# Kernel tuning notes

Hardware: AMD Instinct MI355X
Metric: run time of the kernel (lower is better)

## Reference

```python
import jax, jax.numpy as jnp
import numpy as np

B, C, H, W = 8, 64, 256, 256
V = H * W
E = (H - 1) * W + H * (W - 1)  # vertical + horizontal grid edges
N_ROUNDS = int(np.ceil(np.log2(V)))  # Boruvka halves #components per round


def build_index():
    # matches _build_matrix_index: raw_index[y, x] = y * W + x
    raw = jnp.arange(V, dtype=jnp.int32).reshape(H, W)
    row_e = jnp.stack([raw[:-1, :], raw[1:, :]], axis=-1).reshape(-1, 2)  # vertical edges
    col_e = jnp.stack([raw[:, :-1], raw[:, 1:]], axis=-1).reshape(-1, 2)  # horizontal edges
    return jnp.concatenate([row_e, col_e], axis=0)  # [E, 2]


def edge_weights(fm):
    # distance_func = squared L2 over channel dim; weight = dist + 1 (so weight >= 1)
    b = fm.shape[0]
    d_row = ((fm[:, :, :-1, :] - fm[:, :, 1:, :]) ** 2).sum(1).reshape(b, -1)
    d_col = ((fm[:, :, :, :-1] - fm[:, :, :, 1:]) ** 2).sum(1).reshape(b, -1)
    return jnp.concatenate([d_row, d_col], axis=1) + 1.0  # [B, E]


def mst_boruvka(u, v, w):
    """Parallel Boruvka MST on a connected graph. u, v: [E] int32, w: [E] float32.
    Returns boolean selection mask over edges (exactly V-1 True)."""
    eidx = jnp.arange(E, dtype=jnp.int32)
    vidx = jnp.arange(V, dtype=jnp.int32)
    INF = jnp.float32(jnp.inf)
    BIG = jnp.int32(E)  # sentinel edge id

    def round_fn(state, _):
        comp, sel = state
        cu, cv = comp[u], comp[v]
        active = cu != cv
        wa = jnp.where(active, w, INF)
        # min outgoing edge weight per component
        minw = jnp.full((V,), INF, jnp.float32).at[cu].min(wa).at[cv].min(wa)
        # tie-break by smallest edge index (consistent tie-break -> no long cycles)
        cand_u = jnp.where(active & (wa == minw[cu]), eidx, BIG)
        cand_v = jnp.where(active & (wa == minw[cv]), eidx, BIG)
        best = jnp.full((V,), BIG, jnp.int32).at[cu].min(cand_u).at[cv].min(cand_v)
        has = best < BIG
        be = jnp.clip(best, 0, E - 1)
        cu_b, cv_b = comp[u[be]], comp[v[be]]
        # hook each component onto the component at the other end of its best edge
        parent = jnp.where(has, jnp.where(cu_b == vidx, cv_b, cu_b), vidx)
        # break mutual 2-cycles: keep the smaller label as root
        pp = parent[parent]
        parent = jnp.where((pp == vidx) & (vidx < parent), vidx, parent)
        # pointer jumping to full path compression
        for _ in range(N_ROUNDS):
            parent = parent[parent]
        comp = parent[comp]
        sel = sel.at[jnp.where(has, best, BIG)].set(True, mode='drop')
        return (comp, sel), None

    init = (vidx, jnp.zeros((E,), dtype=bool))
    (comp, sel), _ = jax.lax.scan(round_fn, init, None, length=N_ROUNDS)
    return sel


def setup_inputs() -> dict:
    key = jax.random.key(0)
    guide_in = jax.random.normal(key, (B, C, H, W), dtype=jnp.float32)
    return {"guide_in": guide_in}


def reference(guide_in):
    index = build_index()                      # [E, 2] shared across batch
    weight = edge_weights(guide_in)            # [B, E]
    u, v = index[:, 0], index[:, 1]
    sel = jax.vmap(lambda wb: mst_boruvka(u, v, wb))(weight)  # [B, E] bool
    # grid graph is connected -> exactly V-1 MST edges per image (static shape)
    eids = jax.vmap(lambda s: jnp.nonzero(s, size=V - 1, fill_value=0)[0])(sel)
    tree = index[eids]                         # [B, V-1, 2] vertex pairs of the MST
    return tree
```

## Files before the change

kernel.cpp:

```cpp
#include <hip/hip_runtime.h>
#include <stdint.h>

typedef unsigned long long ull;

#define Bc 8
#define Cc 64
#define Hc 256
#define Wc 256
#define Vc (Hc*Wc)
#define REc ((Hc-1)*Wc)
#define Ec (REc + Hc*(Wc-1))
#define VM1 (Vc-1)
#define INF64 0xFFFFFFFFFFFFFFFFull
#define NRND 16
#define EPB 8192
#define BPB 16

__device__ __forceinline__ void edge_uv(int e, int& u, int& v){
  if (e < REc){ u = e; v = e + Wc; }
  else { int k = e - REc; int i = k / (Wc-1); int j = k - i*(Wc-1); u = i*Wc + j; v = u + 1; }
}

__device__ __forceinline__ ull packw(float w, int e){
  return ((ull)__float_as_uint(w) << 32) | (unsigned)e;
}

__device__ __forceinline__ int chase(const int* __restrict__ parB, int x){
  int p = parB[x];
  while (p != x){ x = p; p = parB[x]; }
  return x;
}

__global__ void __launch_bounds__(1024)
k_weights(const float* __restrict__ g, float* __restrict__ wf,
          int* __restrict__ L, int* __restrict__ par,
          ull* __restrict__ b0, ull* __restrict__ b1,
          unsigned char* __restrict__ sel, int* __restrict__ act, int* __restrict__ outp){
  int t = blockIdx.x*1024 + threadIdx.x;
  int b = t >> 16; int v = t & VM1;
  int i = v >> 8, j = v & (Wc-1);
  const bool hU = i > 0, hD = i < Hc-1, hL = j > 0, hR = j < Wc-1;
  const int oU = hU ? -Wc : 0, oD = hD ? Wc : 0, oL = hL ? -1 : 0, oR = hR ? 1 : 0;
  const float* p = g + (size_t)b*Cc*Vc + v;
  float sU = 0.f, sD = 0.f, sL = 0.f, sR = 0.f;
  #pragma unroll 4
  for (int c = 0; c < Cc; ++c){
    const float* pc = p + (size_t)c*Vc;
    float x = pc[0];
    float dU = x - pc[oU];  float dD = x - pc[oD];
    float dL = x - pc[oL];  float dR = x - pc[oR];
    sU += dU*dU; sD += dD*dD; sL += dL*dL; sR += dR*dR;
  }
  float wU = sU + 1.0f, wD = sD + 1.0f, wL = sL + 1.0f, wR = sR + 1.0f;
  int eU = v - Wc, eD = v, eL = REc + i*(Wc-1) + j - 1, eR = REc + i*(Wc-1) + j;
  ull m = INF64;
  if (hU){ ull x = packw(wU, eU); if (x < m) m = x; }
  if (hD){ ull x = packw(wD, eD); if (x < m) m = x; }
  if (hL){ ull x = packw(wL, eL); if (x < m) m = x; }
  if (hR){ ull x = packw(wR, eR); if (x < m) m = x; }
  b0[t] = m;
  b1[t] = INF64;
  L[t] = v; par[t] = v;
  float* wfb = wf + (size_t)b*Ec;
  unsigned char* selb = sel + (size_t)b*Ec;
  if (hD){ wfb[eD] = wD; selb[eD] = 0; }
  if (hR){ wfb[eR] = wR; selb[eR] = 0; }
  if (t < Bc*VM1){ outp[2*t] = 0; outp[2*t+1] = Wc; }
  if (t < (NRND+2)*Bc) act[t] = 0;
}

__global__ void __launch_bounds__(1024)
k_scanmerge(const float* __restrict__ wf, int* __restrict__ L,
            const int* __restrict__ par,
            ull* __restrict__ bcur, ull* __restrict__ bnxt,
            const int* __restrict__ act, int r){
  int t = blockIdx.x*1024 + threadIdx.x;
  int b = t >> 16;
  if (!act[r*Bc + b]) return;
  int v = t & VM1; const int base = b << 16;
  const int* parB = par + base;
  int Lt0 = L[t];
  int i = v >> 8, j = v & (Wc-1);
  int Lu = (i > 0)    ? L[base + v - Wc] : Lt0;
  int Ld = (i < Hc-1) ? L[base + v + Wc] : Lt0;
  int Ll = (j > 0)    ? L[base + v - 1 ] : Lt0;
  int Lr = (j < Wc-1) ? L[base + v + 1 ] : Lt0;
  if ((Lu==Lt0) & (Ld==Lt0) & (Ll==Lt0) & (Lr==Lt0)){
    if (Lt0 != v) return;
    if (parB[v] == v){ bnxt[t] = INF64; return; }
  }
  int rt = chase(parB, Lt0);
  if (rt != Lt0) L[t] = rt;
  if (v == rt) bnxt[t] = INF64;
  const float* wfb = wf + (size_t)b*Ec;
  ull m = INF64;
  if (Lu != Lt0 && Lu != rt && chase(parB, Lu) != rt){
    int e = v - Wc; ull x = packw(wfb[e], e); if (x < m) m = x; }
  if (Ld != Lt0 && Ld != rt && chase(parB, Ld) != rt){
    int e = v;      ull x = packw(wfb[e], e); if (x < m) m = x; }
  if (Ll != Lt0 && Ll != rt && chase(parB, Ll) != rt){
    int e = REc + i*(Wc-1) + j - 1; ull x = packw(wfb[e], e); if (x < m) m = x; }
  if (Lr != Lt0 && Lr != rt && chase(parB, Lr) != rt){
    int e = REc + i*(Wc-1) + j;     ull x = packw(wfb[e], e); if (x < m) m = x; }
  if (m != INF64) atomicMin(&bcur[base + rt], m);
}

__global__ void __launch_bounds__(1024)
k_hook(const int* __restrict__ L, const ull* __restrict__ bcur,
       int* __restrict__ par, unsigned char* __restrict__ sel, int* __restrict__ act, int r){
  int t = blockIdx.x*1024 + threadIdx.x;
  int b = t >> 16;
  if (r > 0 && !act[r*Bc + b]) return;
  int v = t & VM1;
  if (L[t] != v) return;
  const int base = b << 16;
  ull p = bcur[t];
  int pr = v;
  if (p != INF64){
    int e = (int)(unsigned)p; int eu, ev; edge_uv(e, eu, ev);
    int cu = L[base + eu], cv = L[base + ev];
    int other = (cu == v) ? cv : cu;
    sel[(size_t)b*Ec + e] = 1;
    if (act[(r+1)*Bc + b] == 0) act[(r+1)*Bc + b] = 1;
    pr = (bcur[base + other] == p && v < other) ? v : other;
  }
  par[t] = pr;
}

__global__ void __launch_bounds__(1024)
k_cnt(const unsigned char* __restrict__ sel, int* __restrict__ blkcnt){
  int blk = blockIdx.x; int bb = blk / BPB; int kb = blk % BPB;
  int base = kb*EPB;
  int off = threadIdx.x * 8;
  int c = 0;
  if (base + off < Ec){
    const unsigned int* p = (const unsigned int*)(sel + (size_t)bb*Ec + base + off);
    unsigned int s = p[0] + p[1];
    c = (s & 0xFF) + ((s>>8)&0xFF) + ((s>>16)&0xFF) + (s>>24);
  }
  int lane = threadIdx.x & 63, wave = threadIdx.x >> 6;
  #pragma unroll
  for (int o = 32; o; o >>= 1) c += __shfl_down(c, o, 64);
  __shared__ int sw[16];
  if (lane == 0) sw[wave] = c;
  __syncthreads();
  if (threadIdx.x == 0){
    int s = 0;
    #pragma unroll
    for (int w = 0; w < 16; ++w) s += sw[w];
    blkcnt[blk] = s;
  }
}

__global__ void __launch_bounds__(1024)
k_scatter(const unsigned char* __restrict__ sel, const int* __restrict__ blkcnt,
          int* __restrict__ outp){
  int blk = blockIdx.x; int bb = blk / BPB; int kb = blk % BPB;
  __shared__ int s_boff;
  if (threadIdx.x < 64){
    int c = ((int)threadIdx.x < kb) ? blkcnt[bb*BPB + threadIdx.x] : 0;
    #pragma unroll
    for (int o = 32; o; o >>= 1) c += __shfl_down(c, o, 64);
    if (threadIdx.x == 0) s_boff = c;
  }
  int base = kb*EPB;
  int off = threadIdx.x * 8;
  unsigned int a = 0, d = 0; int c = 0;
  if (base + off < Ec){
    const unsigned int* p = (const unsigned int*)(sel + (size_t)bb*Ec + base + off);
    a = p[0]; d = p[1];
    unsigned int s = a + d;
    c = (s & 0xFF) + ((s>>8)&0xFF) + ((s>>16)&0xFF) + (s>>24);
  }
  int lane = threadIdx.x & 63, wave = threadIdx.x >> 6;
  int x = c;
  #pragma unroll
  for (int o = 1; o < 64; o <<= 1){ int y = __shfl_up(x, o, 64); if (lane >= o) x += y; }
  __shared__ int sw[16];
  if (lane == 63) sw[wave] = x;
  __syncthreads();
  int woff = 0;
  #pragma unroll
  for (int w = 0; w < 16; ++w) if (w < wave) woff += sw[w];
  int pos = s_boff + woff + x - c;
  if (base + off < Ec){
    int* ob = outp + (size_t)bb*VM1*2;
    int ebase = base + off;
    #pragma unroll
    for (int k = 0; k < 8; ++k){
      unsigned int byte = ((k < 4) ? (a >> (8*k)) : (d >> (8*(k-4)))) & 0xFF;
      if (byte){ int e = ebase + k; int u, v; edge_uv(e, u, v); ob[2*pos] = u; ob[2*pos+1] = v; ++pos; }
    }
  }
}

extern "C" void kernel_launch(void* const* d_in, const int* in_sizes, int n_in,
                              void* d_out, int out_size, void* d_ws, size_t ws_size,
                              hipStream_t stream) {
  const float* g = (const float*)d_in[0];
  int* outp = (int*)d_out;

  char* ws = (char*)d_ws;
  size_t off = 0;
  auto alloc = [&](size_t bytes) -> void* {
    void* p = ws + off; off += (bytes + 511) & ~(size_t)511; return p;
  };
  ull* b0 = (ull*)alloc((size_t)Bc*Vc*8);
  ull* b1 = (ull*)alloc((size_t)Bc*Vc*8);
  float* wf = (float*)alloc((size_t)Bc*Ec*4);
  int* L   = (int*)alloc((size_t)Bc*Vc*4);
  int* par = (int*)alloc((size_t)Bc*Vc*4);
  unsigned char* sel = (unsigned char*)alloc((size_t)Bc*Ec);
  int* act  = (int*)alloc((size_t)(NRND+2)*Bc*4);
  int* blkcnt = (int*)alloc((size_t)Bc*BPB*4);

  const int gv = (Bc*Vc)/1024;

  k_weights<<<gv, 1024, 0, stream>>>(g, wf, L, par, b0, b1, sel, act, outp);
  k_hook   <<<gv, 1024, 0, stream>>>(L, b0, par, sel, act, 0);
  for (int r = 1; r < NRND; ++r){
    ull* bcur = (r & 1) ? b1 : b0;
    ull* bnxt = (r & 1) ? b0 : b1;
    k_scanmerge<<<gv, 1024, 0, stream>>>(wf, L, par, bcur, bnxt, act, r);
    k_hook     <<<gv, 1024, 0, stream>>>(L, bcur, par, sel, act, r);
  }
  k_cnt    <<<Bc*BPB, 1024, 0, stream>>>(sel, blkcnt);
  k_scatter<<<Bc*BPB, 1024, 0, stream>>>(sel, blkcnt, outp);
}
```

Before: 248.3 us.

## Fuse edge weighting with tile-local Boruvka rounds in shared memory

Replaces the weight kernel and the first global hook with one kernel. Each 1024-thread block covers a 32x32 tile, computes its edge weights, then runs Boruvka rounds inside shared memory, hooking only when a component's minimum incident edge lies fully inside the tile. Each image enters the global scan/hook rounds with far fewer components, so those rounds do less pointer chasing and fewer atomics, and the act flags let idle rounds exit early. In exchange it adds up to 16 barrier-synchronised local rounds per block and more shared-memory traffic in the first kernel.

Result: faster. 240.8 us (-3.0%).

```diff
diff --git a/kernel.cpp b/kernel.cpp
--- a/kernel.cpp
+++ b/kernel.cpp
@@ -2,6 +2,7 @@
 #include <stdint.h>
 
 typedef unsigned long long ull;
+typedef unsigned short u16;
 
 #define Bc 8
 #define Cc 64
@@ -12,6 +13,7 @@
 #define Ec (REc + Hc*(Wc-1))
 #define VM1 (Vc-1)
 #define INF64 0xFFFFFFFFFFFFFFFFull
+#define TS 32
 #define NRND 16
 #define EPB 8192
 #define BPB 16
@@ -32,41 +34,95 @@
 }
 
 __global__ void __launch_bounds__(1024)
-k_weights(const float* __restrict__ g, float* __restrict__ wf,
-          int* __restrict__ L, int* __restrict__ par,
-          ull* __restrict__ b0, ull* __restrict__ b1,
-          unsigned char* __restrict__ sel, int* __restrict__ act, int* __restrict__ outp){
-  int t = blockIdx.x*1024 + threadIdx.x;
-  int b = t >> 16; int v = t & VM1;
-  int i = v >> 8, j = v & (Wc-1);
+k_stage1(const float* __restrict__ g, float* __restrict__ wf,
+         int* __restrict__ L, int* __restrict__ par, ull* __restrict__ b1,
+         unsigned char* __restrict__ sel, int* __restrict__ act, int* __restrict__ outp){
+  const int blk = blockIdx.x;
+  const int b = blk >> 6, tile = blk & 63;
+  const int ty = tile >> 3, tx = tile & 7;
+  const int tid = threadIdx.x;
+  const int li = tid >> 5, lj = tid & 31;
+  const int i = ty*TS + li, j = tx*TS + lj;
+  const int v = (i << 8) | j;
+
   const bool hU = i > 0, hD = i < Hc-1, hL = j > 0, hR = j < Wc-1;
   const int oU = hU ? -Wc : 0, oD = hD ? Wc : 0, oL = hL ? -1 : 0, oR = hR ? 1 : 0;
   const float* p = g + (size_t)b*Cc*Vc + v;
-  float sU = 0.f, sD = 0.f, sL = 0.f, sR = 0.f;
+  float sU=0.f, sD=0.f, sL=0.f, sR=0.f;
   #pragma unroll 4
   for (int c = 0; c < Cc; ++c){
     const float* pc = p + (size_t)c*Vc;
     float x = pc[0];
-    float dU = x - pc[oU];  float dD = x - pc[oD];
-    float dL = x - pc[oL];  float dR = x - pc[oR];
+    float dU = x - pc[oU]; float dD = x - pc[oD];
+    float dL = x - pc[oL]; float dR = x - pc[oR];
     sU += dU*dU; sD += dD*dD; sL += dL*dL; sR += dR*dR;
   }
-  float wU = sU + 1.0f, wD = sD + 1.0f, wL = sL + 1.0f, wR = sR + 1.0f;
-  int eU = v - Wc, eD = v, eL = REc + i*(Wc-1) + j - 1, eR = REc + i*(Wc-1) + j;
-  ull m = INF64;
-  if (hU){ ull x = packw(wU, eU); if (x < m) m = x; }
-  if (hD){ ull x = packw(wD, eD); if (x < m) m = x; }
-  if (hL){ ull x = packw(wL, eL); if (x < m) m = x; }
-  if (hR){ ull x = packw(wR, eR); if (x < m) m = x; }
-  b0[t] = m;
-  b1[t] = INF64;
-  L[t] = v; par[t] = v;
+  const int eU = v - Wc, eD = v, eL = REc + i*(Wc-1) + j - 1, eR = REc + i*(Wc-1) + j;
+  const ull pU = packw(sU+1.f, eU), pD = packw(sD+1.f, eD);
+  const ull pL = packw(sL+1.f, eL), pR = packw(sR+1.f, eR);
   float* wfb = wf + (size_t)b*Ec;
   unsigned char* selb = sel + (size_t)b*Ec;
-  if (hD){ wfb[eD] = wD; selb[eD] = 0; }
-  if (hR){ wfb[eR] = wR; selb[eR] = 0; }
-  if (t < Bc*VM1){ outp[2*t] = 0; outp[2*t+1] = Wc; }
-  if (t < (NRND+2)*Bc) act[t] = 0;
+  if (hD){ wfb[eD] = sD+1.f; selb[eD] = 0; }
+  if (hR){ wfb[eR] = sR+1.f; selb[eR] = 0; }
+  { int gt = blk*1024 + tid;
+    if (gt < Bc*VM1){ outp[2*gt] = 0; outp[2*gt+1] = Wc; }
+    if (gt < (NRND+2)*Bc) act[gt] = (gt >= Bc && gt < 2*Bc) ? 1 : 0;
+  }
+
+  __shared__ u16 lab[1024];
+  __shared__ u16 spar[1024];
+  __shared__ ull best[1024];
+  __shared__ int s_any;
+  lab[tid] = (u16)tid;
+
+  for (int round = 0; round < 16; ++round){
+    best[tid] = INF64;
+    if (tid == 0) s_any = 0;
+    __syncthreads();
+    int c = lab[tid];
+    ull m = INF64;
+    if (hU){ bool inc = (li > 0)    ? (lab[tid-TS] != c) : true; if (inc && pU < m) m = pU; }
+    if (hD){ bool inc = (li < TS-1) ? (lab[tid+TS] != c) : true; if (inc && pD < m) m = pD; }
+    if (hL){ bool inc = (lj > 0)    ? (lab[tid-1 ] != c) : true; if (inc && pL < m) m = pL; }
+    if (hR){ bool inc = (lj < TS-1) ? (lab[tid+1 ] != c) : true; if (inc && pR < m) m = pR; }
+    if (m != INF64) atomicMin(&best[c], m);
+    __syncthreads();
+    int pr = tid;
+    if (c == tid){
+      ull pb = best[tid];
+      if (pb != INF64){
+        int e = (int)(unsigned)pb; int eu, ev; edge_uv(e, eu, ev);
+        int diu = (eu>>8) - ty*TS, dju = (eu&255) - tx*TS;
+        int div_ = (ev>>8) - ty*TS, djv = (ev&255) - tx*TS;
+        bool inu  = ((unsigned)diu < TS) && ((unsigned)dju < TS);
+        bool inv_ = ((unsigned)div_ < TS) && ((unsigned)djv < TS);
+        if (inu && inv_){
+          int lu = diu*TS + dju, lv = div_*TS + djv;
+          int cu = lab[lu], cv = lab[lv];
+          int other = (cu == tid) ? cv : cu;
+          sel[(size_t)b*Ec + e] = 1;
+          s_any = 1;
+          pr = (best[other] == pb && tid < other) ? tid : other;
+        }
+      }
+    }
+    spar[tid] = (u16)pr;
+    __syncthreads();
+    int x = lab[tid];
+    int pp = spar[x];
+    while (pp != x){ x = pp; pp = spar[x]; }
+    int any = s_any;
+    lab[tid] = (u16)x;
+    __syncthreads();
+    if (!any) break;
+  }
+
+  int rt = lab[tid];
+  int groot = ((ty*TS + (rt>>5)) << 8) | (tx*TS + (rt&31));
+  const int t = (b << 16) | v;
+  L[t] = groot;
+  par[t] = v;
+  b1[t] = INF64;
 }
 
 __global__ void __launch_bounds__(1024)
@@ -110,7 +166,7 @@
        int* __restrict__ par, unsigned char* __restrict__ sel, int* __restrict__ act, int r){
   int t = blockIdx.x*1024 + threadIdx.x;
   int b = t >> 16;
-  if (r > 0 && !act[r*Bc + b]) return;
+  if (!act[r*Bc + b]) return;
   int v = t & VM1;
   if (L[t] != v) return;
   const int base = b << 16;
@@ -216,8 +272,7 @@
 
   const int gv = (Bc*Vc)/1024;
 
-  k_weights<<<gv, 1024, 0, stream>>>(g, wf, L, par, b0, b1, sel, act, outp);
-  k_hook   <<<gv, 1024, 0, stream>>>(L, b0, par, sel, act, 0);
+  k_stage1<<<Bc*64, 1024, 0, stream>>>(g, wf, L, par, b1, sel, act, outp);
   for (int r = 1; r < NRND; ++r){
     ull* bcur = (r & 1) ? b1 : b0;
     ull* bnxt = (r & 1) ? b0 : b1;
```
